# Performance work log

Hardware: AMD Instinct MI355X
Metric: run time of the kernel (lower is better)

## Reference

```python
import jax, jax.numpy as jnp
import numpy as np

MARGIN = 0.3
EPS = 1e-12  # guards sqrt at zero distance (diagonal)


def setup_inputs() -> dict:
    key = jax.random.key(0)
    k1, k2 = jax.random.split(key)
    features = jax.random.normal(k1, (8192, 256), dtype=jnp.float32)
    labels = jax.random.randint(k2, (8192,), 0, 512, dtype=jnp.int64)
    return {"features": features, "labels": labels}


def reference(features, labels):
    # L2 normalize rows (F.normalize default: p=2, dim=1, eps=1e-12)
    norm = jnp.linalg.norm(features, axis=1, keepdims=True)
    f = features / jnp.maximum(norm, 1e-12)

    # pairwise euclidean distances: ||a||^2 + ||b||^2 - 2 a.b, then sqrt
    sq = jnp.sum(f * f, axis=1)  # [N]
    gram = f @ f.T               # [N, N]
    d2 = sq[:, None] + sq[None, :] - 2.0 * gram
    dist = jnp.sqrt(jnp.clip(d2, EPS))  # [N, N]

    mask_pos = labels[:, None] == labels[None, :]  # includes diagonal, as in torch code

    hardest_pos = jnp.max(dist * mask_pos.astype(dist.dtype), axis=1)
    dist_neg = jnp.where(mask_pos, jnp.inf, dist)
    hardest_neg = jnp.min(dist_neg, axis=1)

    loss = jax.nn.relu(hardest_pos - hardest_neg + MARGIN)
    return jnp.mean(loss)
```

## Files before the change

### kernel.cpp

```cpp
#include <hip/hip_runtime.h>
#include <hip/hip_bf16.h>
#include <math.h>

#define N 8192
#define D 256
#define MARGIN 0.3f
#define EPS 1e-12f

#define BT 128
#define NJB (N / BT)
#define TOTAL_TRI (NJB * (NJB + 1) / 2)

typedef __attribute__((ext_vector_type(8))) short short8;
typedef __attribute__((ext_vector_type(4))) float floatx4;

static __device__ inline ushort f2bf(float f) {
    __hip_bfloat16 h = __float2bfloat16(f);
    return *reinterpret_cast<ushort*>(&h);
}


__global__ __launch_bounds__(256) void normalize_kernel(const float* __restrict__ x,
                                                        ushort* __restrict__ fn16t,
                                                        float* __restrict__ out) {
    __shared__ ushort lnorm[16][256];
    const int g    = blockIdx.x;
    const int t    = threadIdx.x;
    const int w    = t >> 6;
    const int lane = t & 63;
    if (g == 0 && t == 0) out[0] = 0.0f;

    #pragma unroll
    for (int rr = 0; rr < 4; rr++) {
        const int rl  = w * 4 + rr;
        const int row = g * 16 + rl;
        float4 v = ((const float4*)(x + (size_t)row * D))[lane];
        float s = v.x * v.x + v.y * v.y + v.z * v.z + v.w * v.w;
        #pragma unroll
        for (int off = 32; off; off >>= 1) s += __shfl_down(s, off);
        s = __shfl(s, 0);
        const float inv = 1.0f / fmaxf(sqrtf(s), 1e-12f);
        ushort4 b;
        b.x = f2bf(v.x * inv); b.y = f2bf(v.y * inv);
        b.z = f2bf(v.z * inv); b.w = f2bf(v.w * inv);
        *(ushort4*)(&lnorm[rl][lane * 4]) = b;
    }
    __syncthreads();
    const int kk = t >> 5;
    const int pp = (t & 31) * 2;
    ushort* base = fn16t + ((size_t)g * 8 + kk) * 512;
    #pragma unroll
    for (int e = 0; e < 2; e++) {
        const int p    = pp + e;
        const int quad = p >> 4;
        const int l15  = p & 15;
        *(short8*)(base + p * 8) = *(const short8*)(&lnorm[l15][kk * 32 + quad * 8]);
    }
}

__global__ __launch_bounds__(256, 3) void gram_kernel(const ushort* __restrict__ fn16t,
                                                      const int* __restrict__ lab,
                                                      float* __restrict__ gp_part,
                                                      float* __restrict__ gn_part) {
    __shared__ float rT[4][BT][17];
    __shared__ float cGp[BT][2], cGn[BT][2];

    const int bidx = blockIdx.x;
    const int idx  = (bidx & 7) * 260 + (bidx >> 3);
    const float c = 2.0f * NJB + 1.0f;
    int ib = (int)((c - sqrtf(c * c - 8.0f * (float)idx)) * 0.5f);
    while (ib > 0 && idx < ib * NJB - ib * (ib - 1) / 2) ib--;
    while (idx >= (ib + 1) * NJB - (ib + 1) * ib / 2) ib++;
    const int jb = ib + (idx - (ib * NJB - ib * (ib - 1) / 2));
    const bool offdiag = (jb > ib);
    const int i0 = ib * BT, j0 = jb * BT;

    const int t    = threadIdx.x;
    const int w    = t >> 6;
    const int lane = t & 63;
    const int wi   = w >> 1, wj = w & 1;
    const int quad = lane >> 4;
    const int l15  = lane & 15;

    const ushort* pA[4];
    const ushort* pB[4];
    #pragma unroll
    for (int m = 0; m < 4; m++)
        pA[m] = fn16t + ((size_t)(ib * 8 + wi * 4 + m)) * 4096 + lane * 8;
    #pragma unroll
    for (int n = 0; n < 4; n++)
        pB[n] = fn16t + ((size_t)(jb * 8 + wj * 4 + n)) * 4096 + lane * 8;

    floatx4 acc[4][4];
    #pragma unroll
    for (int m = 0; m < 4; m++)
        #pragma unroll
        for (int n = 0; n < 4; n++)
            acc[m][n] = (floatx4){0.f, 0.f, 0.f, 0.f};

    #pragma unroll
    for (int kk = 0; kk < 8; kk++) {
        short8 af[4], bf_[4];
        #pragma unroll
        for (int m = 0; m < 4; m++) af[m]  = *(const short8*)(pA[m] + kk * 512);
        #pragma unroll
        for (int n = 0; n < 4; n++) bf_[n] = *(const short8*)(pB[n] + kk * 512);
        #pragma unroll
        for (int m = 0; m < 4; m++)
            #pragma unroll
            for (int n = 0; n < 4; n++)
                acc[m][n] = __builtin_amdgcn_mfma_f32_16x16x32_bf16(af[m], bf_[n], acc[m][n], 0, 0, 0);
    }

    int labj[4];
    #pragma unroll
    for (int n = 0; n < 4; n++) labj[n] = lab[j0 + wj * 64 + n * 16 + l15];
    float gpc[4], gnc[4];
    #pragma unroll
    for (int n = 0; n < 4; n++) { gpc[n] = INFINITY; gnc[n] = -INFINITY; }

    #pragma unroll
    for (int m = 0; m < 4; m++) {
        const int4 li4 = *(const int4*)(lab + i0 + wi * 64 + m * 16 + quad * 4);
        const int labi[4] = {li4.x, li4.y, li4.z, li4.w};
        #pragma unroll
        for (int r = 0; r < 4; r++) {
            float pr = INFINITY, nr = -INFINITY;
            #pragma unroll
            for (int n = 0; n < 4; n++) {
                const float g = acc[m][n][r];
                const bool same = (labi[r] == labj[n]);
                const float selp = same ? g : INFINITY;
                const float seln = same ? -INFINITY : g;
                pr = fminf(pr, selp);           nr = fmaxf(nr, seln);
                gpc[n] = fminf(gpc[n], selp);   gnc[n] = fmaxf(gnc[n], seln);
            }
            if (offdiag) {
                const int irow = wi * 64 + m * 16 + quad * 4 + r;
                rT[(wj << 1) + 0][irow][l15] = pr;
                rT[(wj << 1) + 1][irow][l15] = nr;
            }
        }
    }
    #pragma unroll
    for (int n = 0; n < 4; n++) {
        float p = gpc[n], q2 = gnc[n];
        p  = fminf(p,  __shfl_xor(p, 16));  p  = fminf(p,  __shfl_xor(p, 32));
        q2 = fmaxf(q2, __shfl_xor(q2, 16)); q2 = fmaxf(q2, __shfl_xor(q2, 32));
        if (quad == 0) {
            const int col = wj * 64 + n * 16 + l15;
            cGp[col][wi] = p; cGn[col][wi] = q2;
        }
    }
    __syncthreads();
    if (t < BT) {
        gp_part[(size_t)ib * N + j0 + t] = fminf(cGp[t][0], cGp[t][1]);
        gn_part[(size_t)ib * N + j0 + t] = fmaxf(cGn[t][0], cGn[t][1]);
    } else if (offdiag) {
        const int i = t - BT;
        float p = INFINITY, nn = -INFINITY;
        #pragma unroll
        for (int k = 0; k < 16; k++) {
            p  = fminf(p,  fminf(rT[0][i][k], rT[2][i][k]));
            nn = fmaxf(nn, fmaxf(rT[1][i][k], rT[3][i][k]));
        }
        gp_part[(size_t)jb * N + i0 + i] = p;
        gn_part[(size_t)jb * N + i0 + i] = nn;
    }
}

__global__ __launch_bounds__(256) void reduce_kernel(const float* __restrict__ gp_part,
                                                     const float* __restrict__ gn_part,
                                                     float* __restrict__ out) {
    __shared__ float redp[32][5], redn[32][5];
    const int t  = threadIdx.x;
    const int r  = blockIdx.x * 32 + (t & 31);
    const int sg = t >> 5;
    float gp = INFINITY, gn = -INFINITY;
    #pragma unroll
    for (int q = 0; q < 8; q++) {
        const int s = sg * 8 + q;
        gp = fminf(gp, gp_part[(size_t)s * N + r]);
        gn = fmaxf(gn, gn_part[(size_t)s * N + r]);
    }
    gp = fminf(gp, __shfl_xor(gp, 32));
    gn = fmaxf(gn, __shfl_xor(gn, 32));
    const int w = t >> 6;
    if ((t & 63) < 32) { redp[t & 31][w] = gp; redn[t & 31][w] = gn; }
    __syncthreads();
    if (t < 32) {
        const float p  = fminf(fminf(redp[t][0], redp[t][1]), fminf(redp[t][2], redp[t][3]));
        const float nn = fmaxf(fmaxf(redn[t][0], redn[t][1]), fmaxf(redn[t][2], redn[t][3]));
        const float dp = sqrtf(fmaxf(2.0f - 2.0f * p,  EPS));
        const float dn = sqrtf(fmaxf(2.0f - 2.0f * nn, EPS));
        const float l  = dp - dn + MARGIN;
        float sum = (l > 0.0f) ? l : 0.0f;
        #pragma unroll
        for (int off = 16; off; off >>= 1) sum += __shfl_down(sum, off);
        if (t == 0) atomicAdd(out, sum * (1.0f / (float)N));
    }
}

extern "C" void kernel_launch(void* const* d_in, const int* in_sizes, int n_in,
                              void* d_out, int out_size, void* d_ws, size_t ws_size,
                              hipStream_t stream) {
    const float* x   = (const float*)d_in[0];
    const int*   lab = (const int*)d_in[1];
    float* out = (float*)d_out;

    char* ws = (char*)d_ws;
    ushort* fn16t   = (ushort*)ws;
    float*  gp_part = (float*)(ws + (size_t)N * D * 2);
    float*  gn_part = gp_part + (size_t)NJB * N;

    normalize_kernel<<<N / 16, 256, 0, stream>>>(x, fn16t, out);
    gram_kernel<<<TOTAL_TRI, 256, 0, stream>>>(fn16t, lab, gp_part, gn_part);
    reduce_kernel<<<N / 32, 256, 0, stream>>>(gp_part, gn_part, out);
}
```

Measured before the change: 97.83 us.

## Stage A tile in LDS via global_load_lds and preload all B fragments

The gram kernel now copies the whole 128x256 bf16 A row-block into a 64KB shared buffer with direct global-to-LDS loads, so each A fragment is fetched from global memory once per block instead of once per wave pair. All B fragments for the full K range are loaded into registers up front. The rT reduction scratch is aliased onto the same shared buffer, with an extra barrier before reuse. This raises register and LDS use, so launch bounds drop from 3 to 2 blocks per CU, which lowers occupancy.

```diff
diff --git a/kernel.cpp b/kernel.cpp
--- a/kernel.cpp
+++ b/kernel.cpp
@@ -17,6 +17,12 @@
 static __device__ inline ushort f2bf(float f) {
     __hip_bfloat16 h = __float2bfloat16(f);
     return *reinterpret_cast<ushort*>(&h);
+}
+
+static __device__ inline void gload_lds16(const void* g, void* l) {
+    __builtin_amdgcn_global_load_lds((const __attribute__((address_space(1))) unsigned int*)g,
+                                     (__attribute__((address_space(3))) unsigned int*)l,
+                                     16, 0, 0);
 }
 
 
@@ -58,12 +64,14 @@
     }
 }
 
-__global__ __launch_bounds__(256, 3) void gram_kernel(const ushort* __restrict__ fn16t,
+__global__ __launch_bounds__(256, 2) void gram_kernel(const ushort* __restrict__ fn16t,
                                                       const int* __restrict__ lab,
                                                       float* __restrict__ gp_part,
                                                       float* __restrict__ gn_part) {
-    __shared__ float rT[4][BT][17];
+    __shared__ __attribute__((aligned(16))) char smem[65536];
     __shared__ float cGp[BT][2], cGn[BT][2];
+    ushort* lA = (ushort*)smem;
+    float  (*rT)[BT][17] = (float (*)[BT][17])smem;
 
     const int bidx = blockIdx.x;
     const int idx  = (bidx & 7) * 260 + (bidx >> 3);
@@ -82,14 +90,24 @@
     const int quad = lane >> 4;
     const int l15  = lane & 15;
 
-    const ushort* pA[4];
+    const ushort* gA = fn16t + (size_t)ib * 32768;
+    #pragma unroll
+    for (int c2 = 0; c2 < 16; c2++) {
+        const int cc = w * 16 + c2;
+        gload_lds16(gA + cc * 512 + lane * 8, lA + cc * 512);
+    }
     const ushort* pB[4];
-    #pragma unroll
-    for (int m = 0; m < 4; m++)
-        pA[m] = fn16t + ((size_t)(ib * 8 + wi * 4 + m)) * 4096 + lane * 8;
     #pragma unroll
     for (int n = 0; n < 4; n++)
         pB[n] = fn16t + ((size_t)(jb * 8 + wj * 4 + n)) * 4096 + lane * 8;
+    short8 bfr[8][4];
+    #pragma unroll
+    for (int kk = 0; kk < 8; kk++)
+        #pragma unroll
+        for (int n = 0; n < 4; n++)
+            bfr[kk][n] = *(const short8*)(pB[n] + kk * 512);
+    __builtin_amdgcn_sched_barrier(0);
+    __syncthreads();
 
     floatx4 acc[4][4];
     #pragma unroll
@@ -100,17 +118,17 @@
 
     #pragma unroll
     for (int kk = 0; kk < 8; kk++) {
-        short8 af[4], bf_[4];
-        #pragma unroll
-        for (int m = 0; m < 4; m++) af[m]  = *(const short8*)(pA[m] + kk * 512);
-        #pragma unroll
-        for (int n = 0; n < 4; n++) bf_[n] = *(const short8*)(pB[n] + kk * 512);
+        short8 af[4];
+        #pragma unroll
+        for (int m = 0; m < 4; m++)
+            af[m] = *(const short8*)(lA + (((wi * 4 + m) * 8 + kk) * 512) + lane * 8);
         #pragma unroll
         for (int m = 0; m < 4; m++)
             #pragma unroll
             for (int n = 0; n < 4; n++)
-                acc[m][n] = __builtin_amdgcn_mfma_f32_16x16x32_bf16(af[m], bf_[n], acc[m][n], 0, 0, 0);
-    }
+                acc[m][n] = __builtin_amdgcn_mfma_f32_16x16x32_bf16(af[m], bfr[kk][n], acc[m][n], 0, 0, 0);
+    }
+    __syncthreads();
 
     int labj[4];
     #pragma unroll
```

Result: slower. 101.3 us (+3.5%).

## Process two adjacent column tiles per block to reuse A fragments

Applied to the files above, without the earlier changes.

Each gram block now computes two neighbouring 128x128 upper-triangle tiles in the same row band. The A fragments are loaded once and used for both tiles, and the grid shrinks from 2080 to 1056 blocks. The per-block tile indexing is rewritten as a loop over pair counts per row. The cost is double the accumulator registers, which forces launch bounds down to 2 waves per SIMD, plus an extra barrier between the two epilogues.

```diff
diff --git a/kernel.cpp b/kernel.cpp
--- a/kernel.cpp
+++ b/kernel.cpp
@@ -9,7 +9,7 @@
 
 #define BT 128
 #define NJB (N / BT)
-#define TOTAL_TRI (NJB * (NJB + 1) / 2)
+#define TOTAL_PAIR 1056
 
 typedef __attribute__((ext_vector_type(8))) short short8;
 typedef __attribute__((ext_vector_type(4))) float floatx4;
@@ -58,7 +58,7 @@
     }
 }
 
-__global__ __launch_bounds__(256, 3) void gram_kernel(const ushort* __restrict__ fn16t,
+__global__ __launch_bounds__(256, 2) void gram_kernel(const ushort* __restrict__ fn16t,
                                                       const int* __restrict__ lab,
                                                       float* __restrict__ gp_part,
                                                       float* __restrict__ gn_part) {
@@ -66,14 +66,15 @@
     __shared__ float cGp[BT][2], cGn[BT][2];
 
     const int bidx = blockIdx.x;
-    const int idx  = (bidx & 7) * 260 + (bidx >> 3);
-    const float c = 2.0f * NJB + 1.0f;
-    int ib = (int)((c - sqrtf(c * c - 8.0f * (float)idx)) * 0.5f);
-    while (ib > 0 && idx < ib * NJB - ib * (ib - 1) / 2) ib--;
-    while (idx >= (ib + 1) * NJB - (ib + 1) * ib / 2) ib++;
-    const int jb = ib + (idx - (ib * NJB - ib * (ib - 1) / 2));
-    const bool offdiag = (jb > ib);
-    const int i0 = ib * BT, j0 = jb * BT;
+    int rem = (bidx & 7) * 132 + (bidx >> 3);
+    int ib = 0;
+    while (true) { const int pr = (65 - ib) >> 1; if (rem < pr) break; rem -= pr; ib++; }
+    const int jb0 = ib + 2 * rem;
+    int jb1 = jb0 + 1;
+    const bool has1 = (jb1 < NJB);
+    if (!has1) jb1 = jb0;
+    const bool offdiag0 = (jb0 > ib);
+    const int i0 = ib * BT, j00 = jb0 * BT, j01 = jb1 * BT;
 
     const int t    = threadIdx.x;
     const int w    = t >> 6;
@@ -83,89 +84,118 @@
     const int l15  = lane & 15;
 
     const ushort* pA[4];
-    const ushort* pB[4];
+    const ushort* pB0[4];
+    const ushort* pB1[4];
     #pragma unroll
     for (int m = 0; m < 4; m++)
         pA[m] = fn16t + ((size_t)(ib * 8 + wi * 4 + m)) * 4096 + lane * 8;
     #pragma unroll
-    for (int n = 0; n < 4; n++)
-        pB[n] = fn16t + ((size_t)(jb * 8 + wj * 4 + n)) * 4096 + lane * 8;
-
-    floatx4 acc[4][4];
+    for (int n = 0; n < 4; n++) {
+        pB0[n] = fn16t + ((size_t)(jb0 * 8 + wj * 4 + n)) * 4096 + lane * 8;
+        pB1[n] = fn16t + ((size_t)(jb1 * 8 + wj * 4 + n)) * 4096 + lane * 8;
+    }
+
+    floatx4 acc0[4][4], acc1[4][4];
     #pragma unroll
     for (int m = 0; m < 4; m++)
         #pragma unroll
-        for (int n = 0; n < 4; n++)
-            acc[m][n] = (floatx4){0.f, 0.f, 0.f, 0.f};
+        for (int n = 0; n < 4; n++) {
+            acc0[m][n] = (floatx4){0.f, 0.f, 0.f, 0.f};
+            acc1[m][n] = (floatx4){0.f, 0.f, 0.f, 0.f};
+        }
 
     #pragma unroll
     for (int kk = 0; kk < 8; kk++) {
-        short8 af[4], bf_[4];
-        #pragma unroll
-        for (int m = 0; m < 4; m++) af[m]  = *(const short8*)(pA[m] + kk * 512);
-        #pragma unroll
-        for (int n = 0; n < 4; n++) bf_[n] = *(const short8*)(pB[n] + kk * 512);
+        short8 af[4], b0[4], b1[4];
+        #pragma unroll
+        for (int m = 0; m < 4; m++) af[m] = *(const short8*)(pA[m]  + kk * 512);
+        #pragma unroll
+        for (int n = 0; n < 4; n++) b0[n] = *(const short8*)(pB0[n] + kk * 512);
+        #pragma unroll
+        for (int n = 0; n < 4; n++) b1[n] = *(const short8*)(pB1[n] + kk * 512);
         #pragma unroll
         for (int m = 0; m < 4; m++)
             #pragma unroll
             for (int n = 0; n < 4; n++)
-                acc[m][n] = __builtin_amdgcn_mfma_f32_16x16x32_bf16(af[m], bf_[n], acc[m][n], 0, 0, 0);
-    }
-
-    int labj[4];
-    #pragma unroll
-    for (int n = 0; n < 4; n++) labj[n] = lab[j0 + wj * 64 + n * 16 + l15];
-    float gpc[4], gnc[4];
-    #pragma unroll
-    for (int n = 0; n < 4; n++) { gpc[n] = INFINITY; gnc[n] = -INFINITY; }
-
+                acc0[m][n] = __builtin_amdgcn_mfma_f32_16x16x32_bf16(af[m], b0[n], acc0[m][n], 0, 0, 0);
+        #pragma unroll
+        for (int m = 0; m < 4; m++)
+            #pragma unroll
+            for (int n = 0; n < 4; n++)
+                acc1[m][n] = __builtin_amdgcn_mfma_f32_16x16x32_bf16(af[m], b1[n], acc1[m][n], 0, 0, 0);
+    }
+
+    int labi[4][4];
     #pragma unroll
     for (int m = 0; m < 4; m++) {
         const int4 li4 = *(const int4*)(lab + i0 + wi * 64 + m * 16 + quad * 4);
-        const int labi[4] = {li4.x, li4.y, li4.z, li4.w};
-        #pragma unroll
-        for (int r = 0; r < 4; r++) {
-            float pr = INFINITY, nr = -INFINITY;
+        labi[m][0] = li4.x; labi[m][1] = li4.y; labi[m][2] = li4.z; labi[m][3] = li4.w;
+    }
+
+    #pragma unroll
+    for (int tile = 0; tile < 2; tile++) {
+        const int  jbase   = tile ? j01 : j00;
+        const int  jslot   = tile ? jb1 : jb0;
+        const bool doTile  = tile ? has1 : true;
+        const bool offdiag = tile ? true : offdiag0;
+
+        if (tile) __syncthreads();
+
+        int labj[4];
+        #pragma unroll
+        for (int n = 0; n < 4; n++) labj[n] = lab[jbase + wj * 64 + n * 16 + l15];
+        float gpc[4], gnc[4];
+        #pragma unroll
+        for (int n = 0; n < 4; n++) { gpc[n] = INFINITY; gnc[n] = -INFINITY; }
+
+        #pragma unroll
+        for (int m = 0; m < 4; m++) {
             #pragma unroll
-            for (int n = 0; n < 4; n++) {
-                const float g = acc[m][n][r];
-                const bool same = (labi[r] == labj[n]);
-                const float selp = same ? g : INFINITY;
-                const float seln = same ? -INFINITY : g;
-                pr = fminf(pr, selp);           nr = fmaxf(nr, seln);
-                gpc[n] = fminf(gpc[n], selp);   gnc[n] = fmaxf(gnc[n], seln);
+            for (int r = 0; r < 4; r++) {
+                float pr = INFINITY, nr = -INFINITY;
+                #pragma unroll
+                for (int n = 0; n < 4; n++) {
+                    const float g = tile ? acc1[m][n][r] : acc0[m][n][r];
+                    const bool same = (labi[m][r] == labj[n]);
+                    const float selp = same ? g : INFINITY;
+                    const float seln = same ? -INFINITY : g;
+                    pr = fminf(pr, selp);           nr = fmaxf(nr, seln);
+                    gpc[n] = fminf(gpc[n], selp);   gnc[n] = fmaxf(gnc[n], seln);
+                }
+                if (offdiag) {
+                    const int irow = wi * 64 + m * 16 + quad * 4 + r;
+                    rT[(wj << 1) + 0][irow][l15] = pr;
+                    rT[(wj << 1) + 1][irow][l15] = nr;
+                }
             }
-            if (offdiag) {
-                const int irow = wi * 64 + m * 16 + quad * 4 + r;
-                rT[(wj << 1) + 0][irow][l15] = pr;
-                rT[(wj << 1) + 1][irow][l15] = nr;
+        }
+        #pragma unroll
+        for (int n = 0; n < 4; n++) {
+            float p = gpc[n], q2 = gnc[n];
+            p  = fminf(p,  __shfl_xor(p, 16));  p  = fminf(p,  __shfl_xor(p, 32));
+            q2 = fmaxf(q2, __shfl_xor(q2, 16)); q2 = fmaxf(q2, __shfl_xor(q2, 32));
+            if (quad == 0) {
+                const int col = wj * 64 + n * 16 + l15;
+                cGp[col][wi] = p; cGn[col][wi] = q2;
             }
         }
-    }
-    #pragma unroll
-    for (int n = 0; n < 4; n++) {
-        float p = gpc[n], q2 = gnc[n];
-        p  = fminf(p,  __shfl_xor(p, 16));  p  = fminf(p,  __shfl_xor(p, 32));
-        q2 = fmaxf(q2, __shfl_xor(q2, 16)); q2 = fmaxf(q2, __shfl_xor(q2, 32));
-        if (quad == 0) {
-            const int col = wj * 64 + n * 16 + l15;
-            cGp[col][wi] = p; cGn[col][wi] = q2;
-        }
-    }
-    __syncthreads();
-    if (t < BT) {
-        gp_part[(size_t)ib * N + j0 + t] = fminf(cGp[t][0], cGp[t][1]);
-        gn_part[(size_t)ib * N + j0 + t] = fmaxf(cGn[t][0], cGn[t][1]);
-    } else if (offdiag) {
-        const int i = t - BT;
-        float p = INFINITY, nn = -INFINITY;
-        #pragma unroll
-        for (int k = 0; k < 16; k++) {
-            p  = fminf(p,  fminf(rT[0][i][k], rT[2][i][k]));
-            nn = fmaxf(nn, fmaxf(rT[1][i][k], rT[3][i][k]));
-        }
-        gp_part[(size_t)jb * N + i0 + i] = p;
-        gn_part[(size_t)jb * N + i0 + i] = nn;
+        __syncthreads();
+        if (doTile) {
+            if (t < BT) {
+                gp_part[(size_t)ib * N + jbase + t] = fminf(cGp[t][0], cGp[t][1]);
+                gn_part[(size_t)ib * N + jbase + t] = fmaxf(cGn[t][0], cGn[t][1]);
+            } else if (offdiag) {
+                const int i = t - BT;
+                float p = INFINITY, nn = -INFINITY;
+                #pragma unroll
+                for (int k = 0; k < 16; k++) {
+                    p  = fminf(p,  fminf(rT[0][i][k], rT[2][i][k]));
+                    nn = fmaxf(nn, fmaxf(rT[1][i][k], rT[3][i][k]));
+                }
+                gp_part[(size_t)jslot * N + i0 + i] = p;
+                gn_part[(size_t)jslot * N + i0 + i] = nn;
+            }
+        }
     }
 }
 
@@ -214,6 +244,6 @@
     float*  gn_part = gp_part + (size_t)NJB * N;
 
     normalize_kernel<<<N / 16, 256, 0, stream>>>(x, fn16t, out);
-    gram_kernel<<<TOTAL_TRI, 256, 0, stream>>>(fn16t, lab, gp_part, gn_part);
+    gram_kernel<<<TOTAL_PAIR, 256, 0, stream>>>(fn16t, lab, gp_part, gn_part);
     reduce_kernel<<<N / 32, 256, 0, stream>>>(gp_part, gn_part, out);
 }
```

Measured after the change: 101.4 us. 1.04x slower.
